# Performance work log

Measured on AMD Instinct MI355X. Metric: run time of the kernel, lower is better.

Reference implementation:

```python
import jax, jax.numpy as jnp
import numpy as np
import math

DIM = 1024
N_HEADS = 16
HEAD_DIM = DIM // N_HEADS
FFN_HIDDEN = 4096
EPS = 1e-6


def setup_inputs() -> dict:
    key = jax.random.key(0)
    ks = jax.random.split(key, 10)
    s = 1.0 / math.sqrt(DIM)
    sh = 1.0 / math.sqrt(FFN_HIDDEN)
    return {
        "x": jax.random.normal(ks[0], (2, 2048, DIM), dtype=jnp.float32),
        # attention weights stored as [in, out] (y = x @ W)
        "wq": jax.random.normal(ks[1], (DIM, DIM), dtype=jnp.float32) * s,
        "wk": jax.random.normal(ks[2], (DIM, DIM), dtype=jnp.float32) * s,
        "wv": jax.random.normal(ks[3], (DIM, DIM), dtype=jnp.float32) * s,
        "wo": jax.random.normal(ks[4], (DIM, DIM), dtype=jnp.float32) * s,
        "w_gate": jax.random.normal(ks[5], (DIM, FFN_HIDDEN), dtype=jnp.float32) * s,
        "w_up": jax.random.normal(ks[6], (DIM, FFN_HIDDEN), dtype=jnp.float32) * s,
        "w_down": jax.random.normal(ks[7], (FFN_HIDDEN, DIM), dtype=jnp.float32) * sh,
        "attn_norm_w": jnp.ones((DIM,), dtype=jnp.float32),
        "ffn_norm_w": jnp.ones((DIM,), dtype=jnp.float32),
    }


def rmsnorm(x, w):
    xf = x.astype(jnp.float32)
    rms = jax.lax.rsqrt(jnp.mean(xf * xf, axis=-1, keepdims=True) + EPS)
    return (xf * rms).astype(x.dtype) * w


def attention(x, wq, wk, wv, wo):
    B, T, C = x.shape
    q = (x @ wq).reshape(B, T, N_HEADS, HEAD_DIM)
    k = (x @ wk).reshape(B, T, N_HEADS, HEAD_DIM)
    v = (x @ wv).reshape(B, T, N_HEADS, HEAD_DIM)
    scores = jnp.einsum("bqhd,bkhd->bhqk", q, k) / math.sqrt(HEAD_DIM)
    causal = jnp.tril(jnp.ones((T, T), dtype=bool))  # True = keep
    scores = jnp.where(causal, scores, -jnp.inf)
    attn = jax.nn.softmax(scores, axis=-1)
    out = jnp.einsum("bhqk,bkhd->bqhd", attn, v).reshape(B, T, C)
    return out @ wo


def swiglu(x, w_gate, w_up, w_down):
    return (jax.nn.silu(x @ w_gate) * (x @ w_up)) @ w_down


def reference(x, wq, wk, wv, wo, w_gate, w_up, w_down, attn_norm_w, ffn_norm_w):
    x = x + attention(rmsnorm(x, attn_norm_w), wq, wk, wv, wo)
    x = x + swiglu(rmsnorm(x, ffn_norm_w), w_gate, w_up, w_down)
    return x
```

## Files before the change

### kernel.cpp

```cpp
#include <hip/hip_runtime.h>
#include <hip/hip_bf16.h>
#include <stdint.h>
#include <math.h>

#define DIM   1024
#define TSEQ  2048
#define BATCH 2
#define NH    16
#define HD    64
#define FFN   4096
#define ROWS  (BATCH*TSEQ)
#define QKVN  (3*DIM)

typedef __attribute__((ext_vector_type(8))) short s16x8;
typedef __attribute__((ext_vector_type(4))) float f32x4;

__device__ __forceinline__ unsigned short f2bf(float f) {
  union { float f; unsigned u; } v; v.f = f;
  unsigned r = v.u + 0x7fffu + ((v.u >> 16) & 1u);
  return (unsigned short)(r >> 16);
}
__device__ __forceinline__ float bf2f(unsigned short h) {
  union { unsigned u; float f; } v; v.u = ((unsigned)h) << 16; return v.f;
}
__device__ __forceinline__ unsigned pack_bf2(float lo, float hi) {
  union { float f; unsigned u; } a, c; a.f = lo; c.f = hi;
  return (c.u & 0xffff0000u) | (a.u >> 16);
}

__device__ __forceinline__ void gld16(const void* g, void* l) {
  __builtin_amdgcn_global_load_lds((const __attribute__((address_space(1))) void*)g,
                                   (__attribute__((address_space(3))) void*)l, 16, 0, 0);
}

__device__ __forceinline__ int xcd_swz_flat() {
  const int nx = gridDim.x, ny = gridDim.y;
  const int nwg = nx * ny * gridDim.z;
  const int flat = blockIdx.x + nx * (blockIdx.y + ny * blockIdx.z);
  return (flat & 7) * (nwg >> 3) + (flat >> 3);
}

__global__ void wtrans_k(const float* __restrict__ w, unsigned short* __restrict__ wt,
                         int K, int N, int mode)
{
  __shared__ unsigned short t[64][65];
  const int n0 = blockIdx.x * 64, k0 = blockIdx.y * 64;
  const int tid = threadIdx.x;
  #pragma unroll
  for (int i = 0; i < 16; ++i) {
    const int r = i*4 + (tid >> 6), c = tid & 63;
    t[r][c] = f2bf(w[(size_t)(k0 + r) * N + n0 + c]);
  }
  __syncthreads();
  #pragma unroll
  for (int i = 0; i < 16; ++i) {
    const int r = i*4 + (tid >> 6), c = tid & 63;
    const int n = n0 + r;
    int dr = n;
    if (mode == 1) dr = ((n >> 4) << 5) + (n & 15);
    if (mode == 2) dr = ((n >> 4) << 5) + 16 + (n & 15);
    wt[(size_t)dr * K + k0 + c] = t[c][r];
  }
}

__global__ void wtrans_qkv_k(const float* __restrict__ wq, const float* __restrict__ wk,
                             const float* __restrict__ wv, unsigned short* __restrict__ wt)
{
  __shared__ unsigned short t[64][65];
  const int n0 = blockIdx.x * 64, k0 = blockIdx.y * 64, z = blockIdx.z;
  const float* w = (z == 0) ? wq : (z == 1) ? wk : wv;
  unsigned short* dst = wt + (size_t)z * DIM * DIM;
  const int tid = threadIdx.x;
  #pragma unroll
  for (int i = 0; i < 16; ++i) {
    const int r = i*4 + (tid >> 6), c = tid & 63;
    t[r][c] = f2bf(w[(size_t)(k0 + r) * DIM + n0 + c]);
  }
  __syncthreads();
  #pragma unroll
  for (int i = 0; i < 16; ++i) {
    const int r = i*4 + (tid >> 6), c = tid & 63;
    dst[(size_t)(n0 + r) * DIM + k0 + c] = t[c][r];
  }
}

__global__ void wtrans_gu_k(const float* __restrict__ wg, const float* __restrict__ wu,
                            unsigned short* __restrict__ wt)
{
  __shared__ unsigned short t[64][65];
  const int n0 = blockIdx.x * 64, k0 = blockIdx.y * 64, z = blockIdx.z;
  const float* w = (z == 0) ? wg : wu;
  const int tid = threadIdx.x;
  #pragma unroll
  for (int i = 0; i < 16; ++i) {
    const int r = i*4 + (tid >> 6), c = tid & 63;
    t[r][c] = f2bf(w[(size_t)(k0 + r) * FFN + n0 + c]);
  }
  __syncthreads();
  #pragma unroll
  for (int i = 0; i < 16; ++i) {
    const int r = i*4 + (tid >> 6), c = tid & 63;
    const int n = n0 + r;
    const int dr = ((n >> 4) << 5) + z*16 + (n & 15);
    wt[(size_t)dr * DIM + k0 + c] = t[c][r];
  }
}

__global__ void vtrans_k(const unsigned short* __restrict__ qkv, unsigned short* __restrict__ vt)
{
  __shared__ unsigned short t[64][65];
  const int tt0 = blockIdx.x * 64;
  const int bh = blockIdx.y, b = bh >> 4, h = bh & 15;
  const int tid = threadIdx.x;
  const unsigned short* src = qkv + (size_t)(b*TSEQ + tt0) * QKVN + 2*DIM + h*HD;
  #pragma unroll
  for (int i = 0; i < 16; ++i) {
    const int r = i*4 + (tid >> 6), c = tid & 63;
    t[r][c] = src[(size_t)r * QKVN + c];
  }
  __syncthreads();
  unsigned short* dst = vt + (size_t)bh * HD * TSEQ + tt0;
  #pragma unroll
  for (int i = 0; i < 16; ++i) {
    const int d = i*4 + (tid >> 6), c = tid & 63;
    dst[(size_t)d * TSEQ + c] = t[c][d];
  }
}

__global__ void rmsnorm_k(const float* __restrict__ x, const float* __restrict__ w,
                          unsigned short* __restrict__ o)
{
  const int row = blockIdx.x, tid = threadIdx.x;
  const float4 v = ((const float4*)(x + (size_t)row * DIM))[tid];
  float ss = v.x*v.x + v.y*v.y + v.z*v.z + v.w*v.w;
  #pragma unroll
  for (int off = 32; off >= 1; off >>= 1) ss += __shfl_xor(ss, off);
  __shared__ float sred[4];
  if ((tid & 63) == 0) sred[tid >> 6] = ss;
  __syncthreads();
  const float tot = sred[0] + sred[1] + sred[2] + sred[3];
  const float r = rsqrtf(tot * (1.0f/DIM) + 1e-6f);
  const float4 wv = ((const float4*)w)[tid];
  ushort4 ov;
  ov.x = f2bf(v.x*r*wv.x); ov.y = f2bf(v.y*r*wv.y);
  ov.z = f2bf(v.z*r*wv.z); ov.w = f2bf(v.w*r*wv.w);
  ((ushort4*)(o + (size_t)row * DIM))[tid] = ov;
}

__global__ void rmsnorm3_k(const float* __restrict__ x, const unsigned short* __restrict__ p0,
                           const unsigned short* __restrict__ p1, const float* __restrict__ w,
                           float* __restrict__ x1, unsigned short* __restrict__ o)
{
  const int row = blockIdx.x, tid = threadIdx.x;
  const size_t base = (size_t)row * DIM;
  const float4 a = ((const float4*)(x + base))[tid];
  const ushort4 b = ((const ushort4*)(p0 + base))[tid];
  const ushort4 c = ((const ushort4*)(p1 + base))[tid];
  float4 v;
  v.x = a.x + bf2f(b.x) + bf2f(c.x); v.y = a.y + bf2f(b.y) + bf2f(c.y);
  v.z = a.z + bf2f(b.z) + bf2f(c.z); v.w = a.w + bf2f(b.w) + bf2f(c.w);
  ((float4*)(x1 + base))[tid] = v;
  float ss = v.x*v.x + v.y*v.y + v.z*v.z + v.w*v.w;
  #pragma unroll
  for (int off = 32; off >= 1; off >>= 1) ss += __shfl_xor(ss, off);
  __shared__ float sred[4];
  if ((tid & 63) == 0) sred[tid >> 6] = ss;
  __syncthreads();
  const float tot = sred[0] + sred[1] + sred[2] + sred[3];
  const float r = rsqrtf(tot * (1.0f/DIM) + 1e-6f);
  const float4 wv = ((const float4*)w)[tid];
  ushort4 ov;
  ov.x = f2bf(v.x*r*wv.x); ov.y = f2bf(v.y*r*wv.y);
  ov.z = f2bf(v.z*r*wv.z); ov.w = f2bf(v.w*r*wv.w);
  ((ushort4*)(o + base))[tid] = ov;
}

__global__ void resadd5_k(const float* __restrict__ x1,
                          const unsigned short* __restrict__ q0, const unsigned short* __restrict__ q1,
                          const unsigned short* __restrict__ q2, const unsigned short* __restrict__ q3,
                          float* __restrict__ o)
{
  const size_t i = (size_t)blockIdx.x * 256 + threadIdx.x;
  const float4 a = ((const float4*)x1)[i];
  const ushort4 b = ((const ushort4*)q0)[i];
  const ushort4 c = ((const ushort4*)q1)[i];
  const ushort4 d = ((const ushort4*)q2)[i];
  const ushort4 e = ((const ushort4*)q3)[i];
  float4 v;
  v.x = a.x + bf2f(b.x) + bf2f(c.x) + bf2f(d.x) + bf2f(e.x);
  v.y = a.y + bf2f(b.y) + bf2f(c.y) + bf2f(d.y) + bf2f(e.y);
  v.z = a.z + bf2f(b.z) + bf2f(c.z) + bf2f(d.z) + bf2f(e.z);
  v.w = a.w + bf2f(b.w) + bf2f(c.w) + bf2f(d.w) + bf2f(e.w);
  ((float4*)o)[i] = v;
}

template<int NS>
__global__ void gemm128sp(const unsigned short* __restrict__ A, int lda,
                          const unsigned short* __restrict__ BT, int ldb,
                          unsigned short* __restrict__ P, int ldc, int Ksp)
{
  __shared__ __align__(16) unsigned short lA[128*64];
  __shared__ __align__(16) unsigned short lB[128*64];
  const int nx = gridDim.x, ny = gridDim.y;
  const int w = xcd_swz_flat();
  const int bx = w % nx, by = (w / nx) % ny, bz = w / (nx * ny);
  const int tid = threadIdx.x;
  const int lane = tid & 63;
  const int wid = tid >> 6;
  const int m0 = by * 128, n0 = bx * 128;
  const int Koff = bz * Ksp;
  P += (size_t)bz * ((size_t)ny * 128) * ldc;
  const int wr = (wid >> 1) * 64, wc = (wid & 1) * 64;
  const int lrow = lane & 15, lk8 = (lane >> 4) * 8;

  f32x4 acc[4][4] = {};

  for (int k0 = Koff; k0 < Koff + Ksp; k0 += 64) {
    #pragma unroll
    for (int c = 0; c < 4; ++c) {
      const int boff = c*4096 + tid*16;
      const int row = boff >> 7, colb = boff & 127;
      gld16((const char*)A + ((size_t)(m0+row)*lda + k0)*2 + colb, (char*)lA + boff);
    }
    #pragma unroll
    for (int c = 0; c < 4; ++c) {
      const int boff = c*4096 + tid*16;
      const int row = boff >> 7, colb = boff & 127;
      gld16((const char*)BT + ((size_t)(n0+row)*ldb + k0)*2 + colb, (char*)lB + boff);
    }
    __syncthreads();
    #pragma unroll
    for (int kk = 0; kk < 64; kk += 32) {
      s16x8 af[4], bf[4];
      #pragma unroll
      for (int i = 0; i < 4; ++i) af[i] = *(const s16x8*)&lA[(wr + i*16 + lrow)*64 + kk + lk8];
      #pragma unroll
      for (int j = 0; j < 4; ++j) bf[j] = *(const s16x8*)&lB[(wc + j*16 + lrow)*64 + kk + lk8];
      #pragma unroll
      for (int i = 0; i < 4; ++i)
        #pragma unroll
        for (int j = 0; j < 4; ++j)
          acc[i][j] = __builtin_amdgcn_mfma_f32_16x16x32_bf16(af[i], bf[j], acc[i][j], 0, 0, 0);
    }
    __syncthreads();
  }
  const int er = (lane >> 4) * 4, ec = lane & 15;
  #pragma unroll
  for (int i = 0; i < 4; ++i)
    #pragma unroll
    for (int j = 0; j < 4; ++j) {
      const int gr = m0 + wr + i*16 + er;
      const int gc = n0 + wc + j*16 + ec;
      #pragma unroll
      for (int e = 0; e < 4; ++e)
        P[(size_t)(gr + e) * ldc + gc] = f2bf(acc[i][j][e]);
    }
}

template<int EPI>
__global__ __launch_bounds__(512) void gemm256(const unsigned short* __restrict__ A, int lda,
                                               const unsigned short* __restrict__ BT, int ldb,
                                               void* __restrict__ Cout, int ldc, int K,
                                               int CX, int CY)
{
  __shared__ __align__(16) unsigned short lA[2][256*64];
  __shared__ __align__(16) unsigned short lB[2][256*64];
  const int nx = gridDim.x, ny = gridDim.y;
  const int flat = blockIdx.x + nx * blockIdx.y;
  const int xcd = flat & 7, kk_ = flat >> 3;
  const int RX = nx / CX, RY = ny / CY;
  const int cx = xcd % CX, cy = xcd / CX;
  const int bx = cx * RX + kk_ % RX;
  const int by = cy * RY + kk_ / RX;
  const int tid = threadIdx.x, lane = tid & 63, wid = tid >> 6;
  const int lrow = lane & 15, g = lane >> 4;
  const int wm = wid >> 2, wn = wid & 3;
  const int m0 = by * 256, n0 = bx * 256;

  const int r0 = tid >> 3;
  const int eB = ((r0 >> 5) << 6) | (r0 & 31);
  const int lc0 = ((tid & 7) * 16) ^ ((r0 & 7) << 4);
  const char* pA = (const char*)A + ((size_t)(m0 + r0) * lda) * 2 + lc0;
  const char* pB = (const char*)BT + ((size_t)(n0 + eB) * ldb) * 2 + lc0;
  char* dA = (char*)&lA[0][0] + tid * 16;
  char* dB = (char*)&lB[0][0] + eB * 128 + (tid & 7) * 16;
  const size_t a64 = (size_t)64 * lda * 2;
  const size_t b32 = (size_t)32 * ldb * 2;

#define STG_GA0(t) do { const char* s_ = pA + (size_t)(t) * 128; \
    char* d_ = dA + (((t) & 1) * 32768); \
    gld16(s_, d_); gld16(s_ + 2*a64, d_ + 16384); } while (0)
#define STG_GA1(t) do { const char* s_ = pA + (size_t)(t) * 128 + a64; \
    char* d_ = dA + (((t) & 1) * 32768) + 8192; \
    gld16(s_, d_); gld16(s_ + 2*a64, d_ + 16384); } while (0)
#define STG_GB0(t) do { const char* s_ = pB + (size_t)(t) * 128; \
    char* d_ = dB + (((t) & 1) * 32768); \
    gld16(s_, d_); gld16(s_ + 4*b32, d_ + 16384); } while (0)
#define STG_GB1(t) do { const char* s_ = pB + (size_t)(t) * 128 + b32; \
    char* d_ = dB + (((t) & 1) * 32768) + 4096; \
    gld16(s_, d_); gld16(s_ + 4*b32, d_ + 16384); } while (0)

  const int swz = (lrow & 7) << 4;
  const int c0 = (g * 16) ^ swz;
  const int c1 = c0 ^ 64;
  const char* rdA = (const char*)&lA[0][0] + (wm * 128 + lrow) * 128;
  const char* rdB = (const char*)&lB[0][0] + (wn * 64 + lrow) * 128;

  f32x4 acc[8][4] = {};
  s16x8 a0[4][2], a1[4][2], b0[2][2], b1[2][2];

#define MFMA_Q(rh, ch, AF, BF) do { \
    _Pragma("unroll") \
    for (int i_ = 0; i_ < 4; ++i_) { \
      _Pragma("unroll") \
      for (int j_ = 0; j_ < 2; ++j_) { \
        acc[(rh)*4+i_][(ch)*2+j_] = __builtin_amdgcn_mfma_f32_16x16x32_bf16(AF[i_][0], BF[j_][0], acc[(rh)*4+i_][(ch)*2+j_], 0,0,0); \
        acc[(rh)*4+i_][(ch)*2+j_] = __builtin_amdgcn_mfma_f32_16x16x32_bf16(AF[i_][1], BF[j_][1], acc[(rh)*4+i_][(ch)*2+j_], 0,0,0); \
      } } } while (0)

#define VMCNT(n) asm volatile("s_waitcnt vmcnt(" #n ")" ::: "memory")
#define LGKM0()  do { asm volatile("s_waitcnt lgkmcnt(0)" ::: "memory"); \
                      __builtin_amdgcn_sched_barrier(0); } while (0)
#define BARRIER() do { __builtin_amdgcn_s_barrier(); \
                       __builtin_amdgcn_sched_barrier(0); } while (0)

#define RD_A0(buf) do { _Pragma("unroll") for (int i_ = 0; i_ < 4; ++i_) { \
    a0[i_][0] = *(const s16x8*)((buf) + i_*2048 + c0); \
    a0[i_][1] = *(const s16x8*)((buf) + i_*2048 + c1); } } while (0)
#define RD_A1(buf) do { _Pragma("unroll") for (int i_ = 0; i_ < 4; ++i_) { \
    a1[i_][0] = *(const s16x8*)((buf) + 8192 + i_*2048 + c0); \
    a1[i_][1] = *(const s16x8*)((buf) + 8192 + i_*2048 + c1); } } while (0)
#define RD_B0(buf) do { _Pragma("unroll") for (int j_ = 0; j_ < 2; ++j_) { \
    b0[j_][0] = *(const s16x8*)((buf) + j_*2048 + c0); \
    b0[j_][1] = *(const s16x8*)((buf) + j_*2048 + c1); } } while (0)
#define RD_B1(buf) do { _Pragma("unroll") for (int j_ = 0; j_ < 2; ++j_) { \
    b1[j_][0] = *(const s16x8*)((buf) + 4096 + j_*2048 + c0); \
    b1[j_][1] = *(const s16x8*)((buf) + 4096 + j_*2048 + c1); } } while (0)

#define PRIO_MFMA(rh, ch, AF, BF) do { \
    __builtin_amdgcn_s_setprio(1); MFMA_Q(rh, ch, AF, BF); \
    __builtin_amdgcn_s_setprio(0); } while (0)

  const int NT = K >> 6;

  STG_GA0(0); STG_GB0(0); STG_GB1(0); STG_GA1(0); STG_GA0(1); STG_GB0(1);
  VMCNT(6);
  BARRIER();
  RD_A0(rdA); RD_B0(rdB);

  for (int t = 0; t < NT - 2; ++t) {
    const char* Ac = rdA + (t & 1) * 32768;
    const char* Bc = rdB + (t & 1) * 32768;
    const char* An = rdA + ((t & 1) ^ 1) * 32768;
    const char* Bn = rdB + ((t & 1) ^ 1) * 32768;
    LGKM0();
    RD_B1(Bc); STG_GB1(t + 1);
    PRIO_MFMA(0, 0, a0, b0);
    VMCNT(6); BARRIER();
    LGKM0();
    RD_A1(Ac); STG_GA1(t + 1);
    PRIO_MFMA(0, 1, a0, b1);
    VMCNT(6); BARRIER();
    LGKM0();
    RD_A0(An); STG_GA0(t + 2);
    PRIO_MFMA(1, 0, a1, b0);
    VMCNT(6); BARRIER();
    RD_B0(Bn); STG_GB0(t + 2);
    PRIO_MFMA(1, 1, a1, b1);
    VMCNT(6); BARRIER();
  }
  {
    const char* Ac = rdA;
    const char* Bc = rdB;
    const char* An = rdA + 32768;
    const char* Bn = rdB + 32768;
    LGKM0();
    RD_B1(Bc); STG_GB1(NT - 1);
    PRIO_MFMA(0, 0, a0, b0);
    VMCNT(6); BARRIER();
    LGKM0();
    RD_A1(Ac); STG_GA1(NT - 1);
    PRIO_MFMA(0, 1, a0, b1);
    VMCNT(6); BARRIER();
    LGKM0();
    RD_A0(An);
    PRIO_MFMA(1, 0, a1, b0);
    VMCNT(4); BARRIER();
    RD_B0(Bn);
    PRIO_MFMA(1, 1, a1, b1);
    VMCNT(2); BARRIER();
  }
  {
    const char* Ac = rdA + 32768;
    const char* Bc = rdB + 32768;
    LGKM0();
    RD_B1(Bc);
    PRIO_MFMA(0, 0, a0, b0);
    VMCNT(0); BARRIER();
    LGKM0();
    RD_A1(Ac);
    PRIO_MFMA(0, 1, a0, b1);
    LGKM0();
    PRIO_MFMA(1, 0, a1, b0);
    PRIO_MFMA(1, 1, a1, b1);
  }

  const int er = g * 4, ec = lane & 15;
  if (EPI == 0) {
    unsigned short* C = (unsigned short*)Cout;
    #pragma unroll
    for (int i = 0; i < 8; ++i)
      #pragma unroll
      for (int j = 0; j < 4; ++j) {
        const int gr = m0 + wm*128 + i*16 + er;
        const int gc = n0 + wn*64 + j*16 + ec;
        #pragma unroll
        for (int e = 0; e < 4; ++e)
          C[(size_t)(gr + e) * ldc + gc] = f2bf(acc[i][j][e]);
      }
  } else {
    unsigned short* C = (unsigned short*)Cout;
    #pragma unroll
    for (int i = 0; i < 8; ++i)
      #pragma unroll
      for (int tp = 0; tp < 2; ++tp) {
        const int gr = m0 + wm*128 + i*16 + er;
        const int hc = (n0 >> 1) + wn*32 + tp*16 + ec;
        #pragma unroll
        for (int e = 0; e < 4; ++e) {
          const float gv = acc[i][2*tp][e];
          const float uv = acc[i][2*tp + 1][e];
          const float hv = gv / (1.f + __expf(-gv)) * uv;
          C[(size_t)(gr + e) * ldc + hc] = f2bf(hv);
        }
      }
  }
#undef STG_GA0
#undef STG_GA1
#undef STG_GB0
#undef STG_GB1
#undef MFMA_Q
#undef VMCNT
#undef LGKM0
#undef BARRIER
#undef RD_A0
#undef RD_A1
#undef RD_B0
#undef RD_B1
#undef PRIO_MFMA
}

__global__ __launch_bounds__(512) void attn_fwd(const unsigned short* __restrict__ qkv,
                                                const unsigned short* __restrict__ vt,
                                                unsigned short* __restrict__ outp)
{
  __shared__ __align__(16) unsigned short lK[2][128*64];
  __shared__ __align__(16) unsigned short lV[2][64*128];
  const int nx = gridDim.x;
  const int wsz = xcd_swz_flat();
  const int qblk = wsz % nx;
  const int bh = wsz / nx, b = bh >> 4, h = bh & 15;
  const int tid = threadIdx.x, wid = tid >> 6, lane = tid & 63;
  const int lq = lane & 15, g = lane >> 4;

  const int qrow = qblk*128 + wid*16;
  const int myq = qrow + lq;

  const size_t qbase = ((size_t)(b*TSEQ + myq)) * QKVN + h*HD;
  const s16x8 qf0 = *(const s16x8*)&qkv[qbase + g*8];
  const s16x8 qf1 = *(const s16x8*)&qkv[qbase + 32 + g*8];

  const int pk = tid * 16;
  const int Lk0 = pk ^ (((pk >> 7) & 7) << 4);
  const int Lk1 = (pk + 8192) ^ ((((pk + 8192) >> 7) & 7) << 4);
  const char* ks0 = (const char*)qkv + (((size_t)(b*TSEQ + (Lk0 >> 7))) * QKVN + DIM + h*HD) * 2 + (Lk0 & 127);
  const char* ks1 = (const char*)qkv + (((size_t)(b*TSEQ + (Lk1 >> 7))) * QKVN + DIM + h*HD) * 2 + (Lk1 & 127);
  const int Lv0 = pk ^ (((pk >> 8) & 7) << 4);
  const int Lv1 = (pk + 8192) ^ ((((pk + 8192) >> 8) & 7) << 4);
  const char* vs0 = (const char*)vt + (((size_t)bh*HD + (Lv0 >> 8)) * TSEQ) * 2 + (Lv0 & 255);
  const char* vs1 = (const char*)vt + (((size_t)bh*HD + (Lv1 >> 8)) * TSEQ) * 2 + (Lv1 & 255);

#define STAGE_KV(kt, buf) do { \
    gld16(ks0 + (size_t)(kt)*128*(QKVN*2), (char*)lK[buf] + pk); \
    gld16(ks1 + (size_t)(kt)*128*(QKVN*2), (char*)lK[buf] + pk + 8192); \
    gld16(vs0 + (size_t)(kt)*256,          (char*)lV[buf] + pk); \
    gld16(vs1 + (size_t)(kt)*256,          (char*)lV[buf] + pk + 8192); } while (0)

  float mrun = -INFINITY, lrun = 0.f;
  f32x4 of[4] = {};

  const int nkt = qblk + 1;

  STAGE_KV(0, 0);
  int cur = 0;

  for (int kt = 0; kt < nkt; ++kt) {
    __syncthreads();
    if (kt + 1 < nkt) STAGE_KV(kt + 1, cur ^ 1);
    {
      const char* Kb = (const char*)lK[cur];
      const char* Vb = (const char*)lV[cur];
      f32x4 sacc[8];
      #pragma unroll
      for (int s = 0; s < 8; ++s) {
        const int r = s*16 + lq;
        const int sw = (r & 7) << 4;
        const s16x8 kf0 = *(const s16x8*)(Kb + r*128 + ((g*16) ^ sw));
        const s16x8 kf1 = *(const s16x8*)(Kb + r*128 + ((64 + g*16) ^ sw));
        f32x4 z = {0.f,0.f,0.f,0.f};
        z = __builtin_amdgcn_mfma_f32_16x16x32_bf16(kf0, qf0, z, 0,0,0);
        z = __builtin_amdgcn_mfma_f32_16x16x32_bf16(kf1, qf1, z, 0,0,0);
        sacc[s] = z;
      }
      float p[8][4];
      float mt = -INFINITY;
      #pragma unroll
      for (int s = 0; s < 8; ++s)
        #pragma unroll
        for (int e = 0; e < 4; ++e) {
          const int key = kt*128 + s*16 + 4*g + e;
          const float v = (key <= myq) ? sacc[s][e]*0.125f : -INFINITY;
          p[s][e] = v;
          mt = fmaxf(mt, v);
        }
      mt = fmaxf(mt, __shfl_xor(mt, 16));
      mt = fmaxf(mt, __shfl_xor(mt, 32));
      const float mnew = fmaxf(mrun, mt);
      const float scale = __expf(mrun - mnew);
      float ssum = 0.f;
      #pragma unroll
      for (int s = 0; s < 8; ++s)
        #pragma unroll
        for (int e = 0; e < 4; ++e) {
          p[s][e] = __expf(p[s][e] - mnew);
          ssum += p[s][e];
        }
      ssum += __shfl_xor(ssum, 16);
      ssum += __shfl_xor(ssum, 32);
      lrun = lrun * scale + ssum;
      mrun = mnew;
      #pragma unroll
      for (int d0b = 0; d0b < 4; ++d0b) of[d0b] = of[d0b] * scale;
      #pragma unroll
      for (int hh = 0; hh < 4; ++hh) {
        unsigned w[4];
        #pragma unroll
        for (int j = 0; j < 4; ++j) w[j] = pack_bf2(p[2*hh][j], p[2*hh+1][j]);
        s16x8 bp;
        #pragma unroll
        for (int e = 0; e < 8; ++e) {
          const int srcg = 2*(g & 1) + (e >> 2);
          const unsigned ww = (unsigned)__shfl((int)w[e & 3], lq | (srcg << 4));
          bp[e] = (short)((g >= 2) ? (ww >> 16) : (ww & 0xffffu));
        }
        #pragma unroll
        for (int d0b = 0; d0b < 4; ++d0b) {
          const int r = d0b*16 + lq;
          const int sw = (r & 7) << 4;
          const s16x8 vf = *(const s16x8*)(Vb + r*256 + ((hh*64 + g*16) ^ sw));
          of[d0b] = __builtin_amdgcn_mfma_f32_16x16x32_bf16(vf, bp, of[d0b], 0,0,0);
        }
      }
    }
    cur ^= 1;
  }
  const float inv = 1.f / lrun;
  const size_t obase = ((size_t)(b*TSEQ + myq)) * DIM + h*HD;
  #pragma unroll
  for (int d0b = 0; d0b < 4; ++d0b) {
    ushort4 o;
    o.x = f2bf(of[d0b][0] * inv);
    o.y = f2bf(of[d0b][1] * inv);
    o.z = f2bf(of[d0b][2] * inv);
    o.w = f2bf(of[d0b][3] * inv);
    *(ushort4*)&outp[obase + d0b*16 + 4*g] = o;
  }
#undef STAGE_KV
}

extern "C" void kernel_launch(void* const* d_in, const int* in_sizes, int n_in,
                              void* d_out, int out_size, void* d_ws, size_t ws_size,
                              hipStream_t stream)
{
  const float* x   = (const float*)d_in[0];
  const float* wq  = (const float*)d_in[1];
  const float* wk  = (const float*)d_in[2];
  const float* wv  = (const float*)d_in[3];
  const float* wo  = (const float*)d_in[4];
  const float* wg  = (const float*)d_in[5];
  const float* wu  = (const float*)d_in[6];
  const float* wd  = (const float*)d_in[7];
  const float* anw = (const float*)d_in[8];
  const float* fnw = (const float*)d_in[9];
  float* outp = (float*)d_out;

  const size_t MB = 1024*1024;
  const size_t RD = (size_t)ROWS * DIM;
  char* ws = (char*)d_ws;
  float*          x1    = (float*)         (ws + 0);
  unsigned short* wdT   = (unsigned short*)(ws + 16*MB);
  unsigned short* wguT  = (unsigned short*)(ws + 24*MB);
  unsigned short* wqkvT = (unsigned short*)(ws + 40*MB);
  unsigned short* woT   = (unsigned short*)(ws + 46*MB);
  unsigned short* xn    = (unsigned short*)(ws + 48*MB);
  unsigned short* qkv   = (unsigned short*)(ws + 56*MB);
  unsigned short* vtb   = (unsigned short*)(ws + 80*MB);
  unsigned short* aout  = (unsigned short*)(ws + 88*MB);
  unsigned short* pwo   = (unsigned short*)(ws + 56*MB);
  unsigned short* hbuf  = (unsigned short*)(ws + 56*MB);
  unsigned short* pdn   = (unsigned short*)(ws + 24*MB);

  const dim3 blk(256);

  wtrans_qkv_k<<<dim3(16,16,3), blk, 0, stream>>>(wq, wk, wv, wqkvT);
  wtrans_k<<<dim3(16,16), blk, 0, stream>>>(wo, woT, DIM, DIM, 0);
  wtrans_gu_k<<<dim3(64,16,2), blk, 0, stream>>>(wg, wu, wguT);
  wtrans_k<<<dim3(16,64), blk, 0, stream>>>(wd, wdT, FFN, DIM, 0);

  rmsnorm_k<<<ROWS, blk, 0, stream>>>(x, anw, xn);
  gemm256<0><<<dim3(QKVN/256, ROWS/256), dim3(512), 0, stream>>>(xn, DIM, wqkvT, DIM, qkv, QKVN, DIM, 4, 2);
  vtrans_k<<<dim3(TSEQ/64, BATCH*NH), blk, 0, stream>>>(qkv, vtb);
  attn_fwd<<<dim3(TSEQ/128, BATCH*NH), dim3(512), 0, stream>>>(qkv, vtb, aout);
  gemm128sp<2><<<dim3(DIM/128, ROWS/128, 2), blk, 0, stream>>>(aout, DIM, woT, DIM, pwo, DIM, DIM/2);
  rmsnorm3_k<<<ROWS, blk, 0, stream>>>(x, pwo, pwo + RD, fnw, x1, xn);

  gemm256<2><<<dim3(2*FFN/256, ROWS/256), dim3(512), 0, stream>>>(xn, DIM, wguT, DIM, hbuf, FFN, DIM, 4, 2);
  gemm128sp<4><<<dim3(DIM/128, ROWS/128, 4), blk, 0, stream>>>(hbuf, FFN, wdT, FFN, pdn, DIM, FFN/4);
  resadd5_k<<<dim3(ROWS*DIM/1024), blk, 0, stream>>>(x1, pdn, pdn + RD, pdn + 2*RD, pdn + 3*RD, outp);
}
```

Measured before the change: 292.1 us.

## Merge weight transposes into one launch, add MFMA priority hints, retile QKV GEMM

Folds the four weight-conversion and transpose kernels into a single 4096-block launch that picks its source and destination from the block index, removing three kernel launches. Wraps the attention MFMA sections in s_setprio raises so waves issuing matrix ops get scheduling priority over waves doing softmax. Switches the QKV projection from the 256-tile GEMM to the 128-tile split kernel with a single split, which raises the block count at the cost of less data reuse per block. The gemm128sp<1> instantiation writes bf16 output directly, which has to match what the old path produced.

```diff
diff --git a/kernel.cpp b/kernel.cpp
--- a/kernel.cpp
+++ b/kernel.cpp
@@ -40,11 +40,39 @@
   return (flat & 7) * (nwg >> 3) + (flat >> 3);
 }
 
-__global__ void wtrans_k(const float* __restrict__ w, unsigned short* __restrict__ wt,
-                         int K, int N, int mode)
+__global__ void wtrans_all_k(const float* __restrict__ wq, const float* __restrict__ wk,
+                             const float* __restrict__ wv, const float* __restrict__ wo,
+                             const float* __restrict__ wg, const float* __restrict__ wu,
+                             const float* __restrict__ wd,
+                             unsigned short* __restrict__ wqkvT, unsigned short* __restrict__ woT,
+                             unsigned short* __restrict__ wguT, unsigned short* __restrict__ wdT)
 {
   __shared__ unsigned short t[64][65];
-  const int n0 = blockIdx.x * 64, k0 = blockIdx.y * 64;
+  const int id = blockIdx.x;
+  const float* w; unsigned short* dst; int K, N, mode, n0, k0;
+  if (id < 768) {
+    const int z = id >> 8, rem = id & 255;
+    w = (z == 0) ? wq : (z == 1) ? wk : wv;
+    dst = wqkvT + (size_t)z * 1024 * 1024;
+    K = 1024; N = 1024; mode = 0;
+    n0 = (rem & 15) * 64; k0 = (rem >> 4) * 64;
+  } else if (id < 1024) {
+    const int rem = id - 768;
+    w = wo; dst = woT; K = 1024; N = 1024; mode = 0;
+    n0 = (rem & 15) * 64; k0 = (rem >> 4) * 64;
+  } else if (id < 2048) {
+    const int rem = id - 1024;
+    w = wg; dst = wguT; K = 1024; N = FFN; mode = 1;
+    n0 = (rem & 63) * 64; k0 = (rem >> 6) * 64;
+  } else if (id < 3072) {
+    const int rem = id - 2048;
+    w = wu; dst = wguT; K = 1024; N = FFN; mode = 2;
+    n0 = (rem & 63) * 64; k0 = (rem >> 6) * 64;
+  } else {
+    const int rem = id - 3072;
+    w = wd; dst = wdT; K = FFN; N = 1024; mode = 0;
+    n0 = (rem & 15) * 64; k0 = (rem >> 4) * 64;
+  }
   const int tid = threadIdx.x;
   #pragma unroll
   for (int i = 0; i < 16; ++i) {
@@ -59,50 +87,7 @@
     int dr = n;
     if (mode == 1) dr = ((n >> 4) << 5) + (n & 15);
     if (mode == 2) dr = ((n >> 4) << 5) + 16 + (n & 15);
-    wt[(size_t)dr * K + k0 + c] = t[c][r];
-  }
-}
-
-__global__ void wtrans_qkv_k(const float* __restrict__ wq, const float* __restrict__ wk,
-                             const float* __restrict__ wv, unsigned short* __restrict__ wt)
-{
-  __shared__ unsigned short t[64][65];
-  const int n0 = blockIdx.x * 64, k0 = blockIdx.y * 64, z = blockIdx.z;
-  const float* w = (z == 0) ? wq : (z == 1) ? wk : wv;
-  unsigned short* dst = wt + (size_t)z * DIM * DIM;
-  const int tid = threadIdx.x;
-  #pragma unroll
-  for (int i = 0; i < 16; ++i) {
-    const int r = i*4 + (tid >> 6), c = tid & 63;
-    t[r][c] = f2bf(w[(size_t)(k0 + r) * DIM + n0 + c]);
-  }
-  __syncthreads();
-  #pragma unroll
-  for (int i = 0; i < 16; ++i) {
-    const int r = i*4 + (tid >> 6), c = tid & 63;
-    dst[(size_t)(n0 + r) * DIM + k0 + c] = t[c][r];
-  }
-}
-
-__global__ void wtrans_gu_k(const float* __restrict__ wg, const float* __restrict__ wu,
-                            unsigned short* __restrict__ wt)
-{
-  __shared__ unsigned short t[64][65];
-  const int n0 = blockIdx.x * 64, k0 = blockIdx.y * 64, z = blockIdx.z;
-  const float* w = (z == 0) ? wg : wu;
-  const int tid = threadIdx.x;
-  #pragma unroll
-  for (int i = 0; i < 16; ++i) {
-    const int r = i*4 + (tid >> 6), c = tid & 63;
-    t[r][c] = f2bf(w[(size_t)(k0 + r) * FFN + n0 + c]);
-  }
-  __syncthreads();
-  #pragma unroll
-  for (int i = 0; i < 16; ++i) {
-    const int r = i*4 + (tid >> 6), c = tid & 63;
-    const int n = n0 + r;
-    const int dr = ((n >> 4) << 5) + z*16 + (n & 15);
-    wt[(size_t)dr * DIM + k0 + c] = t[c][r];
+    dst[(size_t)dr * K + k0 + c] = t[c][r];
   }
 }
 
@@ -501,6 +486,7 @@
       const char* Kb = (const char*)lK[cur];
       const char* Vb = (const char*)lV[cur];
       f32x4 sacc[8];
+      __builtin_amdgcn_s_setprio(1);
       #pragma unroll
       for (int s = 0; s < 8; ++s) {
         const int r = s*16 + lq;
@@ -512,6 +498,7 @@
         z = __builtin_amdgcn_mfma_f32_16x16x32_bf16(kf1, qf1, z, 0,0,0);
         sacc[s] = z;
       }
+      __builtin_amdgcn_s_setprio(0);
       float p[8][4];
       float mt = -INFINITY;
       #pragma unroll
@@ -553,6 +540,7 @@
           const unsigned ww = (unsigned)__shfl((int)w[e & 3], lq | (srcg << 4));
           bp[e] = (short)((g >= 2) ? (ww >> 16) : (ww & 0xffffu));
         }
+        __builtin_amdgcn_s_setprio(1);
         #pragma unroll
         for (int d0b = 0; d0b < 4; ++d0b) {
           const int r = d0b*16 + lq;
@@ -560,6 +548,7 @@
           const s16x8 vf = *(const s16x8*)(Vb + r*256 + ((hh*64 + g*16) ^ sw));
           of[d0b] = __builtin_amdgcn_mfma_f32_16x16x32_bf16(vf, bp, of[d0b], 0,0,0);
         }
+        __builtin_amdgcn_s_setprio(0);
       }
     }
     cur ^= 1;
@@ -612,13 +601,11 @@
 
   const dim3 blk(256);
 
-  wtrans_qkv_k<<<dim3(16,16,3), blk, 0, stream>>>(wq, wk, wv, wqkvT);
-  wtrans_k<<<dim3(16,16), blk, 0, stream>>>(wo, woT, DIM, DIM, 0);
-  wtrans_gu_k<<<dim3(64,16,2), blk, 0, stream>>>(wg, wu, wguT);
-  wtrans_k<<<dim3(16,64), blk, 0, stream>>>(wd, wdT, FFN, DIM, 0);
+  wtrans_all_k<<<dim3(4096), blk, 0, stream>>>(wq, wk, wv, wo, wg, wu, wd,
+                                               wqkvT, woT, wguT, wdT);
 
   rmsnorm_k<<<ROWS, blk, 0, stream>>>(x, anw, xn);
-  gemm256<0><<<dim3(QKVN/256, ROWS/256), dim3(512), 0, stream>>>(xn, DIM, wqkvT, DIM, qkv, QKVN, DIM, 4, 2);
+  gemm128sp<1><<<dim3(QKVN/128, ROWS/128, 1), blk, 0, stream>>>(xn, DIM, wqkvT, DIM, qkv, QKVN, DIM);
   vtrans_k<<<dim3(TSEQ/64, BATCH*NH), blk, 0, stream>>>(qkv, vtb);
   attn_fwd<<<dim3(TSEQ/128, BATCH*NH), dim3(512), 0, stream>>>(qkv, vtb, aout);
   gemm128sp<2><<<dim3(DIM/128, ROWS/128, 2), blk, 0, stream>>>(aout, DIM, woT, DIM, pwo, DIM, DIM/2);
```

Result: faster. 285.5 us, median of 2 (-2.3%).
